# Performance work log

Measured on AMD Instinct MI355X. Metric: run time of the kernel, lower is better.

## Reference

```python
import jax, jax.numpy as jnp
import numpy as np

B, H, W, DIM = 8, 64, 64, 256
HEADS, DH = 8, 64
HID = HEADS * DH  # 512
EPS = 1e-5


def setup_inputs() -> dict:
    key = jax.random.key(0)
    k0, k1, k2 = jax.random.split(key, 3)
    return {
        "x": jax.random.normal(k0, (B, H, W, DIM), dtype=jnp.float32),
        "w_qkv": jax.random.normal(k1, (DIM, 3 * HID), dtype=jnp.float32) / np.sqrt(DIM),
        "gn_scale": jnp.ones((HID,), jnp.float32),
        "gn_bias": jnp.zeros((HID,), jnp.float32),
        "w_out": jax.random.normal(k2, (HID, DIM), dtype=jnp.float32) / np.sqrt(HID),
        "b_out": jnp.zeros((DIM,), jnp.float32),
    }


def reference(x, w_qkv, gn_scale, gn_bias, w_out, b_out):
    b, h, w, c = x.shape
    n = h * w
    scale = DH ** -0.5
    # 1x1 conv (no bias) == channel matmul
    qkv = jnp.einsum('bxyc,cf->bxyf', x, w_qkv)
    q, k, v = jnp.split(qkv, 3, axis=-1)
    # 'b x y (h c) -> b h c (x y)'
    to_heads = lambda t: t.reshape(b, n, HEADS, DH).transpose(0, 2, 3, 1)
    q, k, v = map(to_heads, (q, k, v))  # [b, heads, d, n]
    q = jax.nn.softmax(q, axis=-2) * scale  # softmax over feature dim d
    k = jax.nn.softmax(k, axis=-1)          # softmax over token dim n
    context = jnp.einsum('bhdn,bhen->bhde', k, v)   # small d x e context
    out = jnp.einsum('bhde,bhdn->bhen', context, q)  # [b, heads, e, n]
    # 'b h c (x y) -> b x y (h c)'
    out = out.transpose(0, 3, 1, 2).reshape(b, h, w, HID)
    # GroupNorm with 1 group: normalize over (H, W, C) per sample
    mu = out.mean(axis=(1, 2, 3), keepdims=True)
    var = out.var(axis=(1, 2, 3), keepdims=True)
    out = (out - mu) * jax.lax.rsqrt(var + EPS) * gn_scale + gn_bias
    # final 1x1 conv with bias
    return jnp.einsum('bxyf,fc->bxyc', out, w_out) + b_out
```

## Files before the change

kernel.cpp:

```cpp
#include <hip/hip_runtime.h>


typedef unsigned short ushort_t;
typedef __attribute__((ext_vector_type(8))) short short8;
typedef __attribute__((ext_vector_type(4))) float floatx4;

__device__ __forceinline__ float b2f(ushort_t u) {
  unsigned int i = ((unsigned int)u) << 16;
  float f;
  __builtin_memcpy(&f, &i, 4);
  return f;
}
__device__ __forceinline__ ushort_t f2b(float f) {
  unsigned int i;
  __builtin_memcpy(&i, &f, 4);
  unsigned int r = (i + 0x7FFFu + ((i >> 16) & 1u)) >> 16;
  return (ushort_t)r;
}

__device__ __forceinline__ void load_lds16(const ushort_t* g, ushort_t* l) {
  __builtin_amdgcn_global_load_lds(
      (const __attribute__((address_space(1))) unsigned int*)g,
      (__attribute__((address_space(3))) unsigned int*)l, 16, 0, 0);
}

__global__ __launch_bounds__(256) void cast_f32_bf16(
    const float* __restrict__ in, ushort_t* __restrict__ out) {
  long i = ((long)blockIdx.x * 256 + threadIdx.x) * 4;
  float4 v = *(const float4*)(in + i);
  ushort4 o;
  o.x = f2b(v.x);
  o.y = f2b(v.y);
  o.z = f2b(v.z);
  o.w = f2b(v.w);
  *(ushort4*)(out + i) = o;
}

__global__ __launch_bounds__(256) void transpose_f32_bf16(
    const float* __restrict__ in, ushort_t* __restrict__ out, int R, int C,
    const float* __restrict__ scale) {
  __shared__ ushort_t t[32][33];
  int c0 = blockIdx.x * 32, r0 = blockIdx.y * 32;
  int tx = threadIdx.x & 31, ty = threadIdx.x >> 5;
  for (int i = 0; i < 32; i += 8) {
    float s = scale ? scale[r0 + ty + i] : 1.0f;
    t[ty + i][tx] = f2b(in[(long)(r0 + ty + i) * C + c0 + tx] * s);
  }
  __syncthreads();
  for (int i = 0; i < 32; i += 8)
    out[(long)(c0 + ty + i) * R + r0 + tx] = t[tx][ty + i];
}

__global__ __launch_bounds__(64) void prep_gw_kernel(
    const float* __restrict__ gn_scale, const float* __restrict__ gn_bias,
    const float* __restrict__ w_out, const float* __restrict__ b_out,
    float* __restrict__ gw1, float* __restrict__ bias2) {
  int c = blockIdx.x * 64 + threadIdx.x;
  float g1 = 0.f, b2 = 0.f;
  for (int f = 0; f < 512; ++f) {
    float w = w_out[f * 256 + c];
    g1 += gn_scale[f] * w;
    b2 += gn_bias[f] * w;
  }
  gw1[c] = g1;
  bias2[c] = b2 + b_out[c];
}

template <int MODE, bool SWAP>
__global__ __launch_bounds__(256) void gemm_tpl(
    const ushort_t* __restrict__ A, const ushort_t* __restrict__ Bt,
    void* __restrict__ Cv, int M, int K, int F,
    const float* __restrict__ murs, const float* __restrict__ gw1,
    const float* __restrict__ bias2) {
  __shared__ __align__(16) ushort_t As[128][32];
  __shared__ __align__(16) ushort_t Bs[128][32];
  int tid = threadIdx.x;
  long m0 = (long)(SWAP ? blockIdx.y : blockIdx.x) * 128;
  long f0 = (long)(SWAP ? blockIdx.x : blockIdx.y) * 128;
  int wv = tid >> 6, lane = tid & 63;
  int wm = wv & 1, wf = wv >> 1;
  int l15 = lane & 15, quad = lane >> 4;

  floatx4 acc[4][4];
  floatx4 zero = {0.f, 0.f, 0.f, 0.f};
  for (int i = 0; i < 4; i++)
    for (int j = 0; j < 4; j++) acc[i][j] = zero;

  for (int k0 = 0; k0 < K; k0 += 32) {
    __syncthreads();
#pragma unroll
    for (int r = 0; r < 2; ++r) {
      int chunk = r * 256 + tid;
      int row = chunk >> 2;
      int kc = chunk & 3;
      load_lds16(A + (m0 + row) * (long)K + k0 + kc * 8, &As[row][kc * 8]);
      load_lds16(Bt + (f0 + row) * (long)K + k0 + kc * 8, &Bs[row][kc * 8]);
    }
    __syncthreads();
    short8 af[4], bfr[4];
#pragma unroll
    for (int mt = 0; mt < 4; mt++)
      af[mt] = *(const short8*)(&As[wm * 64 + mt * 16 + l15][quad * 8]);
#pragma unroll
    for (int ft = 0; ft < 4; ft++)
      bfr[ft] = *(const short8*)(&Bs[wf * 64 + ft * 16 + l15][quad * 8]);
#pragma unroll
    for (int mt = 0; mt < 4; mt++)
#pragma unroll
      for (int ft = 0; ft < 4; ft++)
        acc[mt][ft] = __builtin_amdgcn_mfma_f32_16x16x32_bf16(
            af[mt], bfr[ft], acc[mt][ft], 0, 0, 0);
  }

  if constexpr (MODE == 1) {
    ushort_t* C = (ushort_t*)Cv;
    bool isk = (m0 < 512);
#pragma unroll
    for (int mt = 0; mt < 4; mt++)
#pragma unroll
      for (int ft = 0; ft < 4; ft++) {
        long col = f0 + wf * 64 + ft * 16 + l15;
#pragma unroll
        for (int r = 0; r < 4; r++) {
          long row = m0 + wm * 64 + mt * 16 + quad * 4 + r;
          float v = acc[mt][ft][r];
          if (isk) v = __expf(v);
          C[row * F + col] = f2b(v);
        }
      }
  } else {
    float* C = (float*)Cv;
    int b = (int)(m0 >> 12);
    float mu = murs[b * 2], rs = murs[b * 2 + 1];
#pragma unroll
    for (int mt = 0; mt < 4; mt++)
#pragma unroll
      for (int ft = 0; ft < 4; ft++) {
        long col = f0 + wf * 64 + ft * 16 + l15;
        float c1 = bias2[col] - rs * mu * gw1[col];
#pragma unroll
        for (int r = 0; r < 4; r++) {
          long row = m0 + wm * 64 + mt * 16 + quad * 4 + r;
          C[row * F + col] = rs * acc[mt][ft][r] + c1;
        }
      }
  }
}

__global__ __launch_bounds__(256) void ctx_mfma(
    const ushort_t* __restrict__ kvT, float* __restrict__ ctxP,
    float* __restrict__ ksumP) {
  int bh = blockIdx.x, cy = blockIdx.y;
  int b = bh >> 3, h = bh & 7;
  int tid = threadIdx.x, wv = tid >> 6, lane = tid & 63;
  int l15 = lane & 15, quad = lane >> 4;
  __shared__ __align__(16) ushort_t kTs[64 * 128];
  __shared__ __align__(16) ushort_t vTs[64 * 128];
  const ushort_t* kbase = kvT + (long)(h * 64) * 32768 + b * 4096 + cy * 256;
  const ushort_t* vbase = kbase + (long)512 * 32768;

  floatx4 acc[4], acc1;
  floatx4 zero = {0.f, 0.f, 0.f, 0.f};
  for (int i = 0; i < 4; i++) acc[i] = zero;
  acc1 = zero;
  short8 ones;
#pragma unroll
  for (int u = 0; u < 8; ++u) ones[u] = (short)0x3F80;

  int r4 = lane >> 4, c = lane & 15;
  for (int tile = 0; tile < 2; ++tile) {
    __syncthreads();
#pragma unroll
    for (int i = 0; i < 4; ++i) {
      int row = wv * 16 + i * 4 + r4;
      int gc = (c & 8) | ((c ^ row) & 7);
      load_lds16(kbase + (long)row * 32768 + tile * 128 + gc * 8,
                 kTs + (wv * 16 + i * 4) * 128 + lane * 8);
      load_lds16(vbase + (long)row * 32768 + tile * 128 + gc * 8,
                 vTs + (wv * 16 + i * 4) * 128 + lane * 8);
    }
    __syncthreads();
#pragma unroll
    for (int ks = 0; ks < 4; ++ks) {
      int d = wv * 16 + l15;
      int cidx = ks * 4 + quad;
      int sa = (cidx & 8) | ((cidx ^ d) & 7);
      short8 a = *(const short8*)(kTs + d * 128 + sa * 8);
      short8 bf[4];
#pragma unroll
      for (int ft = 0; ft < 4; ++ft) {
        int e = ft * 16 + l15;
        int sb = (cidx & 8) | ((cidx ^ e) & 7);
        bf[ft] = *(const short8*)(vTs + e * 128 + sb * 8);
      }
#pragma unroll
      for (int ft = 0; ft < 4; ++ft)
        acc[ft] = __builtin_amdgcn_mfma_f32_16x16x32_bf16(a, bf[ft], acc[ft],
                                                          0, 0, 0);
      acc1 = __builtin_amdgcn_mfma_f32_16x16x32_bf16(a, ones, acc1, 0, 0, 0);
    }
  }
  float* cb = ctxP + ((long)cy * 64 + bh) * 4096;
#pragma unroll
  for (int ft = 0; ft < 4; ++ft)
#pragma unroll
    for (int r = 0; r < 4; ++r)
      cb[(ft * 16 + l15) * 64 + wv * 16 + quad * 4 + r] = acc[ft][r];
  if (l15 == 0) {
    float* kb = ksumP + ((long)cy * 64 + bh) * 64;
#pragma unroll
    for (int r = 0; r < 4; ++r) kb[wv * 16 + quad * 4 + r] = acc1[r];
  }
}

__global__ __launch_bounds__(256) void reduce_kernel(
    const float* __restrict__ ctxP, const float* __restrict__ ksumP,
    ushort_t* __restrict__ ctxB) {
  int bid = blockIdx.x;
  int bh = bid >> 4;
  int j = (bid & 15) * 256 + threadIdx.x;
  int e = j >> 6, d = j & 63;
  float ks = 0.f;
#pragma unroll
  for (int c = 0; c < 16; ++c) ks += ksumP[((long)c * 64 + bh) * 64 + d];
  float s = 0.f;
#pragma unroll
  for (int c = 0; c < 16; ++c) s += ctxP[((long)c * 64 + bh) * 4096 + j];
  int slot = (d >> 3) ^ (e & 7);
  ctxB[(long)bh * 4096 + e * 64 + slot * 8 + (d & 7)] = f2b(s / ks);
}

__global__ __launch_bounds__(256, 4) void qattn_kernel(
    const ushort_t* __restrict__ xb, const ushort_t* __restrict__ wqT,
    const ushort_t* __restrict__ ctxB, ushort_t* __restrict__ A2,
    float* __restrict__ gstats) {
  __shared__ __align__(16) char lds[32800];
  ushort_t* As = (ushort_t*)lds;
  ushort_t* Bs = (ushort_t*)(lds + 16384);
  ushort_t* P = (ushort_t*)lds;
  float* red = (float*)(lds + 32768);

  int tid = threadIdx.x;
  int bx = blockIdx.x, by = blockIdx.y;
  long m0 = (long)bx * 128;
  long f0 = (long)by * 128;
  int wv = tid >> 6, lane = tid & 63;
  int wm = wv & 1, wf = wv >> 1;
  int l15 = lane & 15, quad = lane >> 4;
  int b = bx >> 5;

  floatx4 acc[4][4];
  floatx4 zero = {0.f, 0.f, 0.f, 0.f};
  for (int i = 0; i < 4; i++)
    for (int j = 0; j < 4; j++) acc[i][j] = zero;

  for (int k0 = 0; k0 < 256; k0 += 64) {
    __syncthreads();
#pragma unroll
    for (int r = 0; r < 4; ++r) {
      int chunk = r * 256 + tid;
      int row = chunk >> 3;
      int kc = chunk & 7;
      int gc = kc ^ (row & 7);
      load_lds16(xb + (m0 + row) * 256 + k0 + gc * 8, As + chunk * 8);
      load_lds16(wqT + (f0 + row) * 256 + k0 + gc * 8, Bs + chunk * 8);
    }
    __syncthreads();
#pragma unroll
    for (int ks = 0; ks < 2; ++ks) {
      short8 af[4], bfr[4];
#pragma unroll
      for (int mt = 0; mt < 4; mt++) {
        int row = wm * 64 + mt * 16 + l15;
        int slot = (ks * 4 + quad) ^ (row & 7);
        af[mt] = *(const short8*)(As + row * 64 + slot * 8);
      }
#pragma unroll
      for (int ft = 0; ft < 4; ft++) {
        int rowb = wf * 64 + ft * 16 + l15;
        int slot = (ks * 4 + quad) ^ (rowb & 7);
        bfr[ft] = *(const short8*)(Bs + rowb * 64 + slot * 8);
      }
#pragma unroll
      for (int mt = 0; mt < 4; mt++)
#pragma unroll
        for (int ft = 0; ft < 4; ft++)
          acc[mt][ft] = __builtin_amdgcn_mfma_f32_16x16x32_bf16(
              af[mt], bfr[ft], acc[mt][ft], 0, 0, 0);
    }
  }

  const ushort_t* cg = ctxB + ((long)(b * 8 + by * 2 + wf)) * 4096;
  short8 cfr0[4];
#pragma unroll
  for (int ft = 0; ft < 4; ++ft) {
    int e = ft * 16 + l15;
    int slot = quad ^ (e & 7);
    cfr0[ft] = *(const short8*)(cg + e * 64 + slot * 8);
  }

  __syncthreads();

  float rs[4][4];
#pragma unroll
  for (int mt = 0; mt < 4; mt++)
#pragma unroll
    for (int r = 0; r < 4; r++) rs[mt][r] = 0.f;
#pragma unroll
  for (int mt = 0; mt < 4; mt++)
#pragma unroll
    for (int ft = 0; ft < 4; ft++)
#pragma unroll
      for (int r = 0; r < 4; r++) {
        float e = __expf(acc[mt][ft][r]);
        acc[mt][ft][r] = e;
        rs[mt][r] += e;
      }
#pragma unroll
  for (int mt = 0; mt < 4; mt++)
#pragma unroll
    for (int r = 0; r < 4; r++) {
      float t = rs[mt][r];
      t += __shfl_xor(t, 1);
      t += __shfl_xor(t, 2);
      t += __shfl_xor(t, 4);
      t += __shfl_xor(t, 8);
      rs[mt][r] = 0.125f / t;
    }

  {
    ushort_t* Pw = P + wf * 8192;
#pragma unroll
    for (int mt = 0; mt < 4; mt++)
#pragma unroll
      for (int ft = 0; ft < 4; ft++) {
        int d = ft * 16 + l15;
#pragma unroll
        for (int r = 0; r < 4; r++) {
          int row = wm * 64 + mt * 16 + quad * 4 + r;
          int slot = (d >> 3) ^ (row & 7);
          Pw[row * 64 + slot * 8 + (d & 7)] = f2b(acc[mt][ft][r] * rs[mt][r]);
        }
      }
  }

  short8 cfr1[4];
#pragma unroll
  for (int ft = 0; ft < 4; ++ft) {
    int e = ft * 16 + l15;
    int slot = (4 + quad) ^ (e & 7);
    cfr1[ft] = *(const short8*)(cg + e * 64 + slot * 8);
  }

  floatx4 o[4][4];
  for (int i = 0; i < 4; i++)
    for (int j = 0; j < 4; j++) o[i][j] = zero;
  {
    const ushort_t* Pr = P + wf * 8192;
    short8 af[4];
#pragma unroll
    for (int mt = 0; mt < 4; mt++) {
      int row = wm * 64 + mt * 16 + l15;
      int slot = quad ^ (row & 7);
      af[mt] = *(const short8*)(Pr + row * 64 + slot * 8);
    }
#pragma unroll
    for (int mt = 0; mt < 4; mt++)
#pragma unroll
      for (int ft = 0; ft < 4; ft++)
        o[mt][ft] = __builtin_amdgcn_mfma_f32_16x16x32_bf16(af[mt], cfr0[ft],
                                                            o[mt][ft], 0, 0,
                                                            0);
#pragma unroll
    for (int mt = 0; mt < 4; mt++) {
      int row = wm * 64 + mt * 16 + l15;
      int slot = (4 + quad) ^ (row & 7);
      af[mt] = *(const short8*)(Pr + row * 64 + slot * 8);
    }
#pragma unroll
    for (int mt = 0; mt < 4; mt++)
#pragma unroll
      for (int ft = 0; ft < 4; ft++)
        o[mt][ft] = __builtin_amdgcn_mfma_f32_16x16x32_bf16(af[mt], cfr1[ft],
                                                            o[mt][ft], 0, 0,
                                                            0);
  }

  float lsum = 0.f, lss = 0.f;
#pragma unroll
  for (int mt = 0; mt < 4; mt++)
#pragma unroll
    for (int ft = 0; ft < 4; ft++) {
      long col = f0 + wf * 64 + ft * 16 + l15;
#pragma unroll
      for (int r = 0; r < 4; r++) {
        long row = m0 + wm * 64 + mt * 16 + quad * 4 + r;
        float v = o[mt][ft][r];
        A2[row * 512 + col] = f2b(v);
        lsum += v;
        lss += v * v;
      }
    }
  for (int s = 32; s > 0; s >>= 1) {
    lsum += __shfl_xor(lsum, s);
    lss += __shfl_xor(lss, s);
  }
  if (lane == 0) {
    red[wv * 2] = lsum;
    red[wv * 2 + 1] = lss;
  }
  __syncthreads();
  if (tid == 0) {
    float a = 0.f, c = 0.f;
    for (int w2 = 0; w2 < 4; w2++) {
      a += red[w2 * 2];
      c += red[w2 * 2 + 1];
    }
    atomicAdd(&gstats[b * 2], a);
    atomicAdd(&gstats[b * 2 + 1], c);
  }
}

__global__ __launch_bounds__(64) void finalize_murs(
    const float* __restrict__ gstats, float* __restrict__ murs) {
  int tid = threadIdx.x;
  if (tid < 8) {
    float cnt = 4096.f * 512.f;
    float mu = gstats[tid * 2] / cnt;
    float var = gstats[tid * 2 + 1] / cnt - mu * mu;
    murs[tid * 2] = mu;
    murs[tid * 2 + 1] = rsqrtf(var + 1e-5f);
  }
}

extern "C" void kernel_launch(void* const* d_in, const int* in_sizes, int n_in,
                              void* d_out, int out_size, void* d_ws,
                              size_t ws_size, hipStream_t stream) {
  const float* x = (const float*)d_in[0];
  const float* w_qkv = (const float*)d_in[1];
  const float* gn_scale = (const float*)d_in[2];
  const float* gn_bias = (const float*)d_in[3];
  const float* w_out = (const float*)d_in[4];
  const float* b_out = (const float*)d_in[5];
  float* out = (float*)d_out;

  char* w = (char*)d_ws;
  ushort_t* kvT = (ushort_t*)(w + 33554432);
  ushort_t* A2 = (ushort_t*)(w + 100663296);
  float* ctxP = (float*)(w + 134217728);
  float* ksumP = (float*)(w + 150994944);
  ushort_t* xb = (ushort_t*)(w + 167772160);
  ushort_t* wqkvT = (ushort_t*)(w + 184549376);
  ushort_t* w2T = (ushort_t*)(w + 185335808);
  ushort_t* ctxB = (ushort_t*)(w + 185630720);
  float* gstats = (float*)(w + 186679296);
  float* murs = (float*)(w + 186695744);
  float* bias2 = (float*)(w + 186695808);
  float* gw1 = (float*)(w + 186696832);

  hipMemsetAsync(gstats, 0, 64, stream);

  cast_f32_bf16<<<8388608 / 4 / 256, 256, 0, stream>>>(x, xb);
  transpose_f32_bf16<<<dim3(1536 / 32, 256 / 32), 256, 0, stream>>>(
      w_qkv, wqkvT, 256, 1536, nullptr);
  transpose_f32_bf16<<<dim3(256 / 32, 512 / 32), 256, 0, stream>>>(
      w_out, w2T, 512, 256, gn_scale);
  prep_gw_kernel<<<4, 64, 0, stream>>>(gn_scale, gn_bias, w_out, b_out, gw1,
                                       bias2);
  gemm_tpl<1, true><<<dim3(256, 8), 256, 0, stream>>>(
      wqkvT + 512 * 256, xb, kvT, 1024, 256, 32768, nullptr, nullptr, nullptr);
  ctx_mfma<<<dim3(64, 16), 256, 0, stream>>>(kvT, ctxP, ksumP);
  reduce_kernel<<<1024, 256, 0, stream>>>(ctxP, ksumP, ctxB);
  qattn_kernel<<<dim3(256, 4), 256, 0, stream>>>(xb, wqkvT, ctxB, A2, gstats);
  finalize_murs<<<1, 64, 0, stream>>>(gstats, murs);
  gemm_tpl<2, false><<<dim3(256, 2), 256, 0, stream>>>(
      A2, w2T, out, 32768, 512, 256, murs, gw1, bias2);
}
```

Baseline: 240.5 us.

## Fuse K/V projection GEMM into context kernel, avoiding kvT round trip

Replaces the separate K/V projection GEMM (which wrote exp(K) and V in bf16 to a 64 MB transposed buffer) and the context MFMA kernel with one kernel. Each block computes K and V for its 128-token tile straight from x and the weights, stages them in LDS, then forms the partial context and k-sum. This removes the global write and re-read of K/V. In exchange, each of the 32 token chunks does less context work and the reduction now sums 32 partials instead of 16.

```diff
diff --git a/kernel.cpp b/kernel.cpp
--- a/kernel.cpp
+++ b/kernel.cpp
@@ -112,23 +112,7 @@
             af[mt], bfr[ft], acc[mt][ft], 0, 0, 0);
   }
 
-  if constexpr (MODE == 1) {
-    ushort_t* C = (ushort_t*)Cv;
-    bool isk = (m0 < 512);
-#pragma unroll
-    for (int mt = 0; mt < 4; mt++)
-#pragma unroll
-      for (int ft = 0; ft < 4; ft++) {
-        long col = f0 + wf * 64 + ft * 16 + l15;
-#pragma unroll
-        for (int r = 0; r < 4; r++) {
-          long row = m0 + wm * 64 + mt * 16 + quad * 4 + r;
-          float v = acc[mt][ft][r];
-          if (isk) v = __expf(v);
-          C[row * F + col] = f2b(v);
-        }
-      }
-  } else {
+  {
     float* C = (float*)Cv;
     int b = (int)(m0 >> 12);
     float mu = murs[b * 2], rs = murs[b * 2 + 1];
@@ -147,69 +131,117 @@
   }
 }
 
-__global__ __launch_bounds__(256) void ctx_mfma(
-    const ushort_t* __restrict__ kvT, float* __restrict__ ctxP,
-    float* __restrict__ ksumP) {
+__global__ __launch_bounds__(256) void kvctx_kernel(
+    const ushort_t* __restrict__ xb, const ushort_t* __restrict__ wqkvT,
+    float* __restrict__ ctxP, float* __restrict__ ksumP) {
+  __shared__ __align__(16) char lds[32768];
+  ushort_t* As = (ushort_t*)lds;
+  ushort_t* Bs = (ushort_t*)(lds + 16384);
+  ushort_t* kTs = (ushort_t*)lds;
+  ushort_t* vTs = (ushort_t*)(lds + 16384);
+
   int bh = blockIdx.x, cy = blockIdx.y;
   int b = bh >> 3, h = bh & 7;
   int tid = threadIdx.x, wv = tid >> 6, lane = tid & 63;
+  int wm = wv & 1, wfk = wv >> 1;
   int l15 = lane & 15, quad = lane >> 4;
-  __shared__ __align__(16) ushort_t kTs[64 * 128];
-  __shared__ __align__(16) ushort_t vTs[64 * 128];
-  const ushort_t* kbase = kvT + (long)(h * 64) * 32768 + b * 4096 + cy * 256;
-  const ushort_t* vbase = kbase + (long)512 * 32768;
-
-  floatx4 acc[4], acc1;
+  long m0 = (long)b * 4096 + cy * 128;
+
+  floatx4 acc[4][4];
   floatx4 zero = {0.f, 0.f, 0.f, 0.f};
-  for (int i = 0; i < 4; i++) acc[i] = zero;
+  for (int i = 0; i < 4; i++)
+    for (int j = 0; j < 4; j++) acc[i][j] = zero;
+
+  for (int k0 = 0; k0 < 256; k0 += 64) {
+    __syncthreads();
+#pragma unroll
+    for (int r = 0; r < 4; ++r) {
+      int chunk = r * 256 + tid;
+      int row = chunk >> 3;
+      int kc = chunk & 7;
+      int gc = kc ^ (row & 7);
+      long arow = (row < 64 ? 512 : 960) + h * 64 + row;
+      load_lds16(wqkvT + arow * 256 + k0 + gc * 8, As + chunk * 8);
+      load_lds16(xb + (m0 + row) * 256 + k0 + gc * 8, Bs + chunk * 8);
+    }
+    __syncthreads();
+#pragma unroll
+    for (int ks = 0; ks < 2; ++ks) {
+      short8 af[4], bfr[4];
+#pragma unroll
+      for (int mt = 0; mt < 4; mt++) {
+        int row = wfk * 64 + mt * 16 + l15;
+        int slot = (ks * 4 + quad) ^ (row & 7);
+        af[mt] = *(const short8*)(As + row * 64 + slot * 8);
+      }
+#pragma unroll
+      for (int ft = 0; ft < 4; ft++) {
+        int rowb = wm * 64 + ft * 16 + l15;
+        int slot = (ks * 4 + quad) ^ (rowb & 7);
+        bfr[ft] = *(const short8*)(Bs + rowb * 64 + slot * 8);
+      }
+#pragma unroll
+      for (int mt = 0; mt < 4; mt++)
+#pragma unroll
+        for (int ft = 0; ft < 4; ft++)
+          acc[mt][ft] = __builtin_amdgcn_mfma_f32_16x16x32_bf16(
+              af[mt], bfr[ft], acc[mt][ft], 0, 0, 0);
+    }
+  }
+  __syncthreads();
+
+  {
+    ushort_t* T = wfk ? vTs : kTs;
+#pragma unroll
+    for (int mt = 0; mt < 4; mt++)
+#pragma unroll
+      for (int ft = 0; ft < 4; ft++) {
+        int n = wm * 64 + ft * 16 + l15;
+        int c = n >> 3, u = n & 7;
+#pragma unroll
+        for (int r = 0; r < 4; r++) {
+          int d = mt * 16 + quad * 4 + r;
+          float v = acc[mt][ft][r];
+          if (!wfk) v = __expf(v);
+          int slot = (c & 8) | ((c ^ d) & 7);
+          T[d * 128 + slot * 8 + u] = f2b(v);
+        }
+      }
+  }
+  __syncthreads();
+
+  floatx4 cacc[4], acc1;
+  for (int i = 0; i < 4; i++) cacc[i] = zero;
   acc1 = zero;
   short8 ones;
 #pragma unroll
   for (int u = 0; u < 8; ++u) ones[u] = (short)0x3F80;
-
-  int r4 = lane >> 4, c = lane & 15;
-  for (int tile = 0; tile < 2; ++tile) {
-    __syncthreads();
-#pragma unroll
-    for (int i = 0; i < 4; ++i) {
-      int row = wv * 16 + i * 4 + r4;
-      int gc = (c & 8) | ((c ^ row) & 7);
-      load_lds16(kbase + (long)row * 32768 + tile * 128 + gc * 8,
-                 kTs + (wv * 16 + i * 4) * 128 + lane * 8);
-      load_lds16(vbase + (long)row * 32768 + tile * 128 + gc * 8,
-                 vTs + (wv * 16 + i * 4) * 128 + lane * 8);
-    }
-    __syncthreads();
-#pragma unroll
-    for (int ks = 0; ks < 4; ++ks) {
-      int d = wv * 16 + l15;
-      int cidx = ks * 4 + quad;
-      int sa = (cidx & 8) | ((cidx ^ d) & 7);
-      short8 a = *(const short8*)(kTs + d * 128 + sa * 8);
-      short8 bf[4];
-#pragma unroll
-      for (int ft = 0; ft < 4; ++ft) {
-        int e = ft * 16 + l15;
-        int sb = (cidx & 8) | ((cidx ^ e) & 7);
-        bf[ft] = *(const short8*)(vTs + e * 128 + sb * 8);
-      }
-#pragma unroll
-      for (int ft = 0; ft < 4; ++ft)
-        acc[ft] = __builtin_amdgcn_mfma_f32_16x16x32_bf16(a, bf[ft], acc[ft],
-                                                          0, 0, 0);
-      acc1 = __builtin_amdgcn_mfma_f32_16x16x32_bf16(a, ones, acc1, 0, 0, 0);
-    }
+#pragma unroll
+  for (int ks = 0; ks < 4; ++ks) {
+    int d = wv * 16 + l15;
+    int cidx = ks * 4 + quad;
+    int sa = (cidx & 8) | ((cidx ^ d) & 7);
+    short8 a = *(const short8*)(kTs + d * 128 + sa * 8);
+    short8 bf[4];
+#pragma unroll
+    for (int ft = 0; ft < 4; ++ft) {
+      int e = ft * 16 + l15;
+      int sb = (cidx & 8) | ((cidx ^ e) & 7);
+      bf[ft] = *(const short8*)(vTs + e * 128 + sb * 8);
+    }
+#pragma unroll
+    for (int ft = 0; ft < 4; ++ft)
+      cacc[ft] = __builtin_amdgcn_mfma_f32_16x16x32_bf16(a, bf[ft], cacc[ft],
+                                                         0, 0, 0);
+    acc1 = __builtin_amdgcn_mfma_f32_16x16x32_bf16(a, ones, acc1, 0, 0, 0);
   }
   float* cb = ctxP + ((long)cy * 64 + bh) * 4096;
 #pragma unroll
   for (int ft = 0; ft < 4; ++ft)
-#pragma unroll
-    for (int r = 0; r < 4; ++r)
-      cb[(ft * 16 + l15) * 64 + wv * 16 + quad * 4 + r] = acc[ft][r];
+    *(floatx4*)&cb[(ft * 16 + l15) * 64 + wv * 16 + quad * 4] = cacc[ft];
   if (l15 == 0) {
     float* kb = ksumP + ((long)cy * 64 + bh) * 64;
-#pragma unroll
-    for (int r = 0; r < 4; ++r) kb[wv * 16 + quad * 4 + r] = acc1[r];
+    *(floatx4*)&kb[wv * 16 + quad * 4] = acc1;
   }
 }
 
@@ -222,10 +254,10 @@
   int e = j >> 6, d = j & 63;
   float ks = 0.f;
 #pragma unroll
-  for (int c = 0; c < 16; ++c) ks += ksumP[((long)c * 64 + bh) * 64 + d];
+  for (int c = 0; c < 32; ++c) ks += ksumP[((long)c * 64 + bh) * 64 + d];
   float s = 0.f;
 #pragma unroll
-  for (int c = 0; c < 16; ++c) s += ctxP[((long)c * 64 + bh) * 4096 + j];
+  for (int c = 0; c < 32; ++c) s += ctxP[((long)c * 64 + bh) * 4096 + j];
   int slot = (d >> 3) ^ (e & 7);
   ctxB[(long)bh * 4096 + e * 64 + slot * 8 + (d & 7)] = f2b(s / ks);
 }
@@ -445,18 +477,17 @@
   float* out = (float*)d_out;
 
   char* w = (char*)d_ws;
-  ushort_t* kvT = (ushort_t*)(w + 33554432);
-  ushort_t* A2 = (ushort_t*)(w + 100663296);
-  float* ctxP = (float*)(w + 134217728);
-  float* ksumP = (float*)(w + 150994944);
-  ushort_t* xb = (ushort_t*)(w + 167772160);
-  ushort_t* wqkvT = (ushort_t*)(w + 184549376);
-  ushort_t* w2T = (ushort_t*)(w + 185335808);
-  ushort_t* ctxB = (ushort_t*)(w + 185630720);
-  float* gstats = (float*)(w + 186679296);
-  float* murs = (float*)(w + 186695744);
-  float* bias2 = (float*)(w + 186695808);
-  float* gw1 = (float*)(w + 186696832);
+  ushort_t* xb = (ushort_t*)(w + 0);
+  ushort_t* A2 = (ushort_t*)(w + 16777216);
+  float* ctxP = (float*)(w + 50331648);
+  float* ksumP = (float*)(w + 83886080);
+  ushort_t* wqkvT = (ushort_t*)(w + 84410368);
+  ushort_t* w2T = (ushort_t*)(w + 85196800);
+  ushort_t* ctxB = (ushort_t*)(w + 85458944);
+  float* gstats = (float*)(w + 85983232);
+  float* murs = (float*)(w + 85983296);
+  float* bias2 = (float*)(w + 85983360);
+  float* gw1 = (float*)(w + 85984384);
 
   hipMemsetAsync(gstats, 0, 64, stream);
 
@@ -467,9 +498,7 @@
       w_out, w2T, 512, 256, gn_scale);
   prep_gw_kernel<<<4, 64, 0, stream>>>(gn_scale, gn_bias, w_out, b_out, gw1,
                                        bias2);
-  gemm_tpl<1, true><<<dim3(256, 8), 256, 0, stream>>>(
-      wqkvT + 512 * 256, xb, kvT, 1024, 256, 32768, nullptr, nullptr, nullptr);
-  ctx_mfma<<<dim3(64, 16), 256, 0, stream>>>(kvT, ctxP, ksumP);
+  kvctx_kernel<<<dim3(64, 32), 256, 0, stream>>>(xb, wqkvT, ctxP, ksumP);
   reduce_kernel<<<1024, 256, 0, stream>>>(ctxP, ksumP, ctxB);
   qattn_kernel<<<dim3(256, 4), 256, 0, stream>>>(xb, wqkvT, ctxB, A2, gstats);
   finalize_murs<<<1, 64, 0, stream>>>(gstats, murs);
```

Result: faster. 230.4 us (-4.2%).
